# Kernel tuning notes

Hardware: AMD Instinct MI355X
Metric: run time of the kernel (lower is better)

## Reference

```python
import jax, jax.numpy as jnp
import numpy as np

D = 20          # embedding dim (hardcoded in original module)
N_REL = 200     # relation vocab size (table has N_REL+1 rows)
N_TIME = 365    # time embedding table size
L = 3           # propagation layers
E = 2_000_000   # edges per layer
N = 1_000_000   # node-slot pool per layer
B = 64          # batch size
N_ENT = 1_000_003


def setup_inputs() -> dict:
    key = jax.random.key(0)
    ks = jax.random.split(key, 16)
    src_idx = jax.random.randint(ks[0], (L, E), 0, N, dtype=jnp.int32)
    dst_idx = jax.random.randint(ks[1], (L, E), 0, N, dtype=jnp.int32)
    rel_idx = jax.random.randint(ks[2], (L, E), 0, N_REL + 1, dtype=jnp.int32)
    qrel_idx = jax.random.randint(ks[3], (L, E), 0, N_REL + 1, dtype=jnp.int32)
    # signed relative time (edge_time - query_time); abs() must stay < N_TIME
    rel_time = jax.random.randint(ks[4], (L, E), -(N_TIME - 1), N_TIME, dtype=jnp.int32)
    node_batch = jax.random.randint(ks[5], (N,), 0, B, dtype=jnp.int32)
    node_ent = jnp.arange(N, dtype=jnp.int32)  # unique entity per final node slot
    s = 0.1
    rela_embed = jax.random.normal(ks[6], (N_REL + 1, D), jnp.float32) * s
    time_embed = jax.random.normal(ks[7], (N_TIME, D), jnp.float32) * s
    w_att1 = jax.random.normal(ks[8], (30, 3 * D), jnp.float32) * s
    w_att2 = jax.random.normal(ks[9], (1, 30), jnp.float32) * s
    w_past = jax.random.normal(ks[10], (D, D), jnp.float32) * s
    w_now = jax.random.normal(ks[11], (D, D), jnp.float32) * s
    w_future = jax.random.normal(ks[12], (D, D), jnp.float32) * s
    w_cls = jax.random.normal(ks[13], (D,), jnp.float32) * s
    b_cls = jnp.zeros((), jnp.float32)
    return dict(src_idx=src_idx, dst_idx=dst_idx, rel_idx=rel_idx,
                qrel_idx=qrel_idx, rel_time=rel_time, node_batch=node_batch,
                node_ent=node_ent, rela_embed=rela_embed, time_embed=time_embed,
                w_att1=w_att1, w_att2=w_att2, w_past=w_past, w_now=w_now,
                w_future=w_future, w_cls=w_cls, b_cls=b_cls,
                batch_size=B, n_ent=N_ENT)


def reference(src_idx, dst_idx, rel_idx, qrel_idx, rel_time, node_batch,
              node_ent, rela_embed, time_embed, w_att1, w_att2, w_past,
              w_now, w_future, w_cls, b_cls, batch_size, n_ent):
    n_layers = src_idx.shape[0]
    n_nodes = node_batch.shape[0]
    d = rela_embed.shape[1]
    hidden = jnp.zeros((n_nodes, d), dtype=rela_embed.dtype)
    for l in range(n_layers):
        rt = rel_time[l]                         # [E] signed relative time
        h_src = hidden[src_idx[l]]               # [E, D] gather
        r_emb = rela_embed[rel_idx[l]]           # [E, D]
        t_emb = time_embed[jnp.abs(rt)]          # [E, D]
        embed_rel = h_src + r_emb + t_emb
        # conditional time-branch MLP (mask-partitioned linear, same math as
        # the original's boolean-masked assignments)
        fut = embed_rel @ w_future.T
        now = embed_rel @ w_now.T
        pst = embed_rel @ w_past.T
        transformed = jnp.where((rt > 0)[:, None], fut,
                       jnp.where((rt == 0)[:, None], now, pst))
        # attention over concat(hidden_src, rel_emb, query_rel_emb)  [E, 3D]
        att_in = jnp.concatenate([h_src, r_emb, rela_embed[qrel_idx[l]]], axis=1)
        score = jax.nn.sigmoid(jax.nn.relu(att_in @ w_att1.T) @ w_att2.T)  # [E,1]
        msg = score * transformed                # [E, D]
        hidden = jax.ops.segment_sum(msg, dst_idx[l], num_segments=n_nodes)
        hidden = jax.nn.leaky_relu(hidden)       # default slope 0.01, as torch
    result = hidden @ w_cls + b_cls              # [N]
    score_all = jnp.zeros((batch_size, n_ent), dtype=result.dtype)
    score_all = score_all.at[node_batch, node_ent].set(result)
    return score_all
```

## Files before the change

kernel.cpp:

```cpp
#include <hip/hip_runtime.h>
#include <hip/hip_bf16.h>
#include <cstdint>

#define DD 20
#define HID 30
#define NB_SCAN 1024
#define MROW 21

typedef unsigned int  u32;
typedef unsigned short u16;

__device__ __forceinline__ void load20(const float* __restrict__ p, float* r){
  const float4* q = (const float4*)p;
#pragma unroll
  for (int i=0;i<5;i++){ float4 v=q[i]; r[4*i+0]=v.x; r[4*i+1]=v.y; r[4*i+2]=v.z; r[4*i+3]=v.w; }
}

__global__ void k_prep(const float* __restrict__ rela, const float* __restrict__ w1,
                       const float* __restrict__ wp, const float* __restrict__ wn,
                       const float* __restrict__ wf,
                       float* __restrict__ W3, float* __restrict__ AR, float* __restrict__ AQ,
                       int nrel){
  int t = blockIdx.x*blockDim.x + threadIdx.x;
  if (t < 3*DD*DD){
    int s = t/(DD*DD), idx = t%(DD*DD);
    W3[t] = (s==0)?wp[idx]:((s==1)?wn[idx]:wf[idx]);
  }
  if (t < nrel*HID){
    int r=t/HID, j=t-r*HID;
    float sr=0.f, sq=0.f;
#pragma unroll
    for (int k=0;k<DD;k++){
      float e = rela[r*DD+k];
      sr += e*w1[j*3*DD + DD + k];
      sq += e*w1[j*3*DD + 2*DD + k];
    }
    AR[r*32+j]=sr; AQ[r*32+j]=sq;
  }
}

__global__ void k_rwtw(const float* __restrict__ rela, const float* __restrict__ timee,
                       const float* __restrict__ W3,
                       float* __restrict__ RW, float* __restrict__ TW,
                       int nrel, int ntime){
  int t = blockIdx.x*blockDim.x+threadIdx.x;
  int totR = 3*nrel*DD, totT = 3*ntime*DD;
  if (t < totR){
    int sel = t/(nrel*DD); int rem = t - sel*nrel*DD; int r = rem/DD; int i = rem - r*DD;
    const float* w = W3 + sel*DD*DD + i*DD;
    const float* e = rela + (size_t)r*DD;
    float s=0.f;
#pragma unroll
    for (int k=0;k<DD;k++) s += e[k]*w[k];
    RW[t]=s;
  }
  if (t < totT){
    int sel = t/(ntime*DD); int rem = t - sel*ntime*DD; int tt = rem/DD; int i = rem - tt*DD;
    const float* w = W3 + sel*DD*DD + i*DD;
    const float* e = timee + (size_t)tt*DD;
    float s=0.f;
#pragma unroll
    for (int k=0;k<DD;k++) s += e[k]*w[k];
    TW[t]=s;
  }
}

__global__ void k_rt(const float* __restrict__ rela, const float* __restrict__ timee,
                     const float* __restrict__ W3, float* __restrict__ RT,
                     int nrel, int ntime){
  int row = blockIdx.x*blockDim.x+threadIdx.x;
  int tot = 3*nrel*ntime;
  if (row>=tot) return;
  int per = nrel*ntime;
  int sel = row/per; int rem = row - sel*per; int r = rem/ntime; int t = rem - r*ntime;
  float e[DD], tv[DD];
  load20(rela + (size_t)r*DD, e);
  load20(timee + (size_t)t*DD, tv);
#pragma unroll
  for (int k=0;k<DD;k++) e[k]+=tv[k];
  const float* W = W3 + sel*DD*DD;
  float o[DD];
#pragma unroll
  for (int i=0;i<DD;i++){
    const float4* wr = (const float4*)(W + i*DD);
    float s=0.f;
#pragma unroll
    for (int c=0;c<5;c++){ float4 w=wr[c]; s += e[4*c]*w.x + e[4*c+1]*w.y + e[4*c+2]*w.z + e[4*c+3]*w.w; }
    o[i]=s;
  }
  float4* op=(float4*)(RT + (size_t)row*DD);
#pragma unroll
  for (int c=0;c<5;c++){ float4 v; v.x=o[4*c]; v.y=o[4*c+1]; v.z=o[4*c+2]; v.w=o[4*c+3]; op[c]=v; }
}

__global__ void __launch_bounds__(256) k_pre(const int* __restrict__ dst, int* __restrict__ cnt,
        int* __restrict__ rank, int E, int N,
        float4* __restrict__ dout4, size_t nd4,
        float4* __restrict__ b0, float4* __restrict__ b1, size_t nb4,
        float4* __restrict__ bF, size_t nf4,
        float4* __restrict__ res4, size_t nr4){
  int g=blockIdx.x, tid=threadIdx.x;
  int half=gridDim.x>>1;
  if (g & 1){
    int stride=half*256;
    int E2=2*E;
    for (int e=(g>>1)*256+tid; e<E2; e+=stride){
      int l=(e>=E)?1:0;
      rank[e]=atomicAdd(&cnt[(size_t)l*N+dst[e]],1);
    }
  } else {
    float4 z=make_float4(0.f,0.f,0.f,0.f);
    size_t i=(size_t)(g>>1)*256+tid, st=(size_t)half*256;
    for (size_t k=i;k<nd4;k+=st) dout4[k]=z;
    for (size_t k=i;k<nb4;k+=st){ b0[k]=z; b1[k]=z; }
    for (size_t k=i;k<nf4;k+=st) bF[k]=z;
    for (size_t k=i;k<nr4;k+=st) res4[k]=z;
  }
}

__global__ void k_scan_part(const int* __restrict__ cnt, int* __restrict__ part, int M, int C){
  __shared__ int sm[256];
  int b=blockIdx.x, t=threadIdx.x;
  int lo=b*C, hi=lo+C; if (hi>M) hi=M; if (lo>M) lo=M;
  int s=0;
  for (int i=lo+t; i<hi; i+=256) s+=cnt[i];
  sm[t]=s; __syncthreads();
  for (int o=128;o>0;o>>=1){ if (t<o) sm[t]+=sm[t+o]; __syncthreads(); }
  if (t==0) part[b]=sm[0];
}

__global__ void k_scan_top(int* __restrict__ part, int* __restrict__ listc){
  __shared__ int sm[NB_SCAN];
  int t=threadIdx.x;
  if (t==0) *listc=0;
  int v=part[t]; sm[t]=v; __syncthreads();
  for (int o=1;o<NB_SCAN;o<<=1){
    int u=(t>=o)?sm[t-o]:0; __syncthreads();
    sm[t]+=u; __syncthreads();
  }
  part[t]=sm[t]-v;
}

__global__ void k_scan_write(const int* __restrict__ cnt, const int* __restrict__ part,
                             int* __restrict__ rowptr, int M, int C, int base){
  __shared__ int sm[256];
  int b=blockIdx.x, t=threadIdx.x;
  int lo=b*C, hi=lo+C; if (hi>M) hi=M; if (lo>M) lo=M;
  int run=part[b]+base;
  for (int bb=lo; bb<hi; bb+=256){
    int i=bb+t;
    int v=(i<hi)?cnt[i]:0;
    sm[t]=v; __syncthreads();
    for (int o=1;o<256;o<<=1){
      int u=(t>=o)?sm[t-o]:0; __syncthreads();
      sm[t]+=u; __syncthreads();
    }
    if (i<hi) rowptr[i]=run+sm[t]-v;
    int tot=sm[255];
    __syncthreads();
    run+=tot;
  }
  if (hi==M && t==0) rowptr[M]=run;
}

__global__ void __launch_bounds__(256) k_scat01(const int* __restrict__ src,const int* __restrict__ dst,
  const int* __restrict__ rel,const int* __restrict__ qrel,const int* __restrict__ rtm,
  const int* __restrict__ rank,const int* __restrict__ rowptr,int4* __restrict__ recs,int E,int N){
  int e=blockIdx.x*blockDim.x+threadIdx.x;
  if (e>=2*E) return;
  int l=(e>=E)?1:0;
  int d=dst[e];
  int pos=rowptr[(size_t)l*N+d]+rank[e];
  recs[pos]=make_int4(src[e], rel[e]|(qrel[e]<<16), rtm[e], d);
}

__global__ void __launch_bounds__(256) k_scat2(const int* __restrict__ src,const int* __restrict__ dst,
  const int* __restrict__ rel,const int* __restrict__ qrel,const int* __restrict__ rtm,
  const int* __restrict__ rank,const int* __restrict__ rowptr2,int4* __restrict__ recs,int E){
  int e=blockIdx.x*blockDim.x+threadIdx.x;
  if (e>=E) return;
  int d=dst[e];
  int pos=rowptr2[d]+rank[e];
  recs[pos]=make_int4(src[e], rel[e]|(qrel[e]<<16), rtm[e], d);
}

template<bool HASH,bool FINAL,bool HIST>
__global__ void __launch_bounds__(256) k_fused(
    const int4* __restrict__ recs,
    const float* __restrict__ hin, float* __restrict__ hout, float* __restrict__ bufF,
    const float* __restrict__ RW, const float* __restrict__ TW,
    const float* __restrict__ AR, const float* __restrict__ AQ,
    const float* __restrict__ w1, const float* __restrict__ w2, const float* __restrict__ W3,
    int E, int nrel, int ntime,
    const int* __restrict__ hB_dst, int* __restrict__ hB_cnt, int* __restrict__ hB_rank, int hB_E,
    const float* __restrict__ wcls, float* __restrict__ res,
    int* __restrict__ list, int* __restrict__ listc)
{
  int lb;
  if (HIST){
    int g=blockIdx.x;
    int r3=g%3, b3=g/3;
    if (r3==2){
      int H=gridDim.x/3;
      int stride=H*256;
      for (int e=b3*256+threadIdx.x; e<hB_E; e+=stride)
        hB_rank[e]=atomicAdd(&hB_cnt[hB_dst[e]],1);
      return;
    }
    lb=b3*2+r3;
  } else lb=blockIdx.x;
  int bstart=lb*256;
  if (bstart>=E) return;

  __shared__ float sW1h[HID*DD];
  __shared__ float sW2[32];
  __shared__ float sW3[3*DD*DD];
  __shared__ float smsg[256*MROW];
  __shared__ int   sdst[256];
  __shared__ int   s_prevdst, s_nextdst;
  if (HASH){
    for (int t=threadIdx.x; t<HID*DD; t+=blockDim.x){ int j=t/DD,k=t-j*DD; sW1h[t]=w1[j*3*DD+k]; }
    for (int t=threadIdx.x; t<3*DD*DD; t+=blockDim.x) sW3[t]=W3[t];
  }
  if (threadIdx.x<HID) sW2[threadIdx.x]=w2[threadIdx.x];

  int tid = threadIdx.x;
  int bsize = E - bstart; if (bsize>256) bsize=256;
  int j = bstart + tid;
  bool active = (tid < bsize);

  if (tid==0){
    s_prevdst = (bstart>0) ? recs[-1 + (ptrdiff_t)bstart].w : -1;
    s_nextdst = (bstart+bsize < E) ? recs[bstart+bsize].w : -1;
  }
  __syncthreads();

  int dstv = -1;
  float m[DD];
  if (active){
    int4 rc = recs[j];
    int s = rc.x;
    int r = rc.y & 0xFFFF;
    int q = ((unsigned)rc.y) >> 16;
    int t = rc.z;
    dstv  = rc.w;
    int sel = (t>0)?2:((t==0)?1:0);
    int ta = (t<0)?-t:t;

    float h[DD];
    if (HASH){
      load20(hin+(size_t)s*DD, h);
#pragma unroll
      for (int i=0;i<DD;i++) h[i]=fmaxf(h[i],0.01f*h[i]);
    }

    float z=0.f;
    {
      const float4* ap=(const float4*)(AR+(size_t)r*32);
      const float4* qp=(const float4*)(AQ+(size_t)q*32);
#pragma unroll
      for (int c=0;c<7;c++){
        float4 x=ap[c], y=qp[c];
        float s4[4]={x.x+y.x, x.y+y.y, x.z+y.z, x.w+y.w};
#pragma unroll
        for (int u=0;u<4;u++){
          int jj=4*c+u;
          if (HASH){
            const float4* wr=(const float4*)&sW1h[jj*DD];
            float sum=s4[u];
#pragma unroll
            for (int c2=0;c2<5;c2++){ float4 w=wr[c2]; sum += h[4*c2]*w.x+h[4*c2+1]*w.y+h[4*c2+2]*w.z+h[4*c2+3]*w.w; }
            s4[u]=sum;
          }
          z += fmaxf(s4[u],0.f)*sW2[jj];
        }
      }
      float2 x2=*(const float2*)(AR+(size_t)r*32+28);
      float2 y2=*(const float2*)(AQ+(size_t)q*32+28);
      float s0=x2.x+y2.x, s1=x2.y+y2.y;
      if (HASH){
        const float4* wr0=(const float4*)&sW1h[28*DD];
        const float4* wr1=(const float4*)&sW1h[29*DD];
#pragma unroll
        for (int c2=0;c2<5;c2++){
          float4 wA=wr0[c2], wB=wr1[c2];
          s0 += h[4*c2]*wA.x+h[4*c2+1]*wA.y+h[4*c2+2]*wA.z+h[4*c2+3]*wA.w;
          s1 += h[4*c2]*wB.x+h[4*c2+1]*wB.y+h[4*c2+2]*wB.z+h[4*c2+3]*wB.w;
        }
      }
      z += fmaxf(s0,0.f)*sW2[28] + fmaxf(s1,0.f)*sW2[29];
    }
    float score = 1.f/(1.f+__expf(-z));

    const float4* rwp=(const float4*)(RW + ((size_t)(sel*nrel+r))*DD);
    const float4* twp=(const float4*)(TW + ((size_t)(sel*ntime+ta))*DD);
#pragma unroll
    for (int c=0;c<5;c++){
      float4 a4=rwp[c], b4=twp[c];
      float mv[4]={a4.x+b4.x, a4.y+b4.y, a4.z+b4.z, a4.w+b4.w};
      if (HASH){
#pragma unroll
        for (int u=0;u<4;u++){
          const float4* wr=(const float4*)&sW3[sel*DD*DD+(4*c+u)*DD];
          float sum=mv[u];
#pragma unroll
          for (int c2=0;c2<5;c2++){ float4 w=wr[c2]; sum += h[4*c2]*w.x+h[4*c2+1]*w.y+h[4*c2+2]*w.z+h[4*c2+3]*w.w; }
          mv[u]=sum;
        }
      }
#pragma unroll
      for (int u=0;u<4;u++){ m[4*c+u]=score*mv[u]; smsg[tid*MROW+4*c+u]=m[4*c+u]; }
    }
  }
  sdst[tid] = active ? dstv : -2;
  __syncthreads();

  if (!active) return;
  bool isHead = (tid==0) ? (s_prevdst != dstv) : (sdst[tid-1] != dstv);
  if (!(isHead || tid==0)) return;
  int k=tid+1;
  for (; k<bsize && sdst[k]==dstv; ++k){
    const float* row=&smsg[k*MROW];
#pragma unroll
    for (int i=0;i<DD;i++) m[i]+=row[i];
  }
  bool crossStart = (tid==0 && !isHead);
  bool crossEnd   = (k==bsize) && (s_nextdst==dstv);
  if (crossStart || crossEnd){
    float* o = bufF + (size_t)dstv*DD;
#pragma unroll
    for (int i=0;i<DD;i++) atomicAdd(o+i, m[i]);
    if (!FINAL && isHead){
      int p = atomicAdd(listc,1);
      list[p] = dstv;
    }
  } else {
    if (!FINAL){
      float4* op=(float4*)(hout + (size_t)dstv*DD);
#pragma unroll
      for (int c=0;c<5;c++){ float4 v; v.x=m[4*c]; v.y=m[4*c+1]; v.z=m[4*c+2]; v.w=m[4*c+3]; op[c]=v; }
    } else {
      float rsum=0.f;
#pragma unroll
      for (int i=0;i<DD;i++){ float x=fmaxf(m[i],0.01f*m[i]); rsum += x*wcls[i]; }
      res[dstv] = rsum;
    }
  }
}

__global__ void __launch_bounds__(256) k_fixup(float* __restrict__ bufF, float* __restrict__ hout,
   const int* __restrict__ list,const int* __restrict__ listc){
  int c=*listc;
  for (int i=blockIdx.x*blockDim.x+threadIdx.x; i<c; i+=gridDim.x*blockDim.x){
    int n=list[i];
    float* p=bufF+(size_t)n*DD;
    float* o=hout+(size_t)n*DD;
#pragma unroll
    for (int jj=0;jj<DD;jj++){ o[jj]=p[jj]; p[jj]=0.f; }
  }
}

__global__ void __launch_bounds__(256) k_out(const float* __restrict__ res,
   const float* __restrict__ bufF, const float* __restrict__ wcls, const float* __restrict__ bcls,
   const int* __restrict__ nb, const int* __restrict__ ne, const int* __restrict__ nentp,
   float* __restrict__ out, int N){
  int n=blockIdx.x*blockDim.x+threadIdx.x;
  if (n>=N) return;
  float acc = res[n] + bcls[0];
  const float4* q=(const float4*)(bufF+(size_t)n*DD);
#pragma unroll
  for (int c=0;c<5;c++){
    float4 v=q[c];
    acc += fmaxf(v.x,0.01f*v.x)*wcls[4*c]   + fmaxf(v.y,0.01f*v.y)*wcls[4*c+1]
         + fmaxf(v.z,0.01f*v.z)*wcls[4*c+2] + fmaxf(v.w,0.01f*v.w)*wcls[4*c+3];
  }
  long long stride = nentp[0];
  out[(long long)nb[n]*stride + ne[n]] = acc;
}

template<bool HASH>
__global__ void __launch_bounds__(256) k_edge(
    const int* __restrict__ src, const int* __restrict__ dst,
    const int* __restrict__ rel, const int* __restrict__ qrel,
    const int* __restrict__ rtm,
    const float* __restrict__ hin, float* __restrict__ hout,
    const float* __restrict__ RT, const float* __restrict__ AR, const float* __restrict__ AQ,
    const float* __restrict__ w1, const float* __restrict__ w2, const float* __restrict__ W3,
    int E, int nrel, int ntime)
{
  __shared__ float sW1h[HID*DD];
  __shared__ float sW2[32];
  __shared__ float sW3[3*DD*DD];
  for (int t=threadIdx.x; t<HID*DD; t+=blockDim.x){ int j=t/DD,k=t-j*DD; sW1h[t]=w1[j*3*DD+k]; }
  if (threadIdx.x<HID) sW2[threadIdx.x]=w2[threadIdx.x];
  for (int t=threadIdx.x; t<3*DD*DD; t+=blockDim.x) sW3[t]=W3[t];
  __syncthreads();
  int e = blockIdx.x*blockDim.x+threadIdx.x;
  if (e>=E) return;
  int s=src[e], d=dst[e], r=rel[e], q=qrel[e], t=rtm[e];
  int sel = (t>0)?2:((t==0)?1:0);
  int ta = (t<0)?-t:t;
  float h[DD];
  if (HASH){
    load20(hin+(size_t)s*DD, h);
#pragma unroll
    for (int i=0;i<DD;i++) h[i]=fmaxf(h[i],0.01f*h[i]);
  }
  float a[HID];
  {
    const float4* ap=(const float4*)(AR+(size_t)r*32);
    const float4* qp=(const float4*)(AQ+(size_t)q*32);
#pragma unroll
    for (int c=0;c<7;c++){
      float4 x=ap[c], y=qp[c];
      a[4*c+0]=x.x+y.x; a[4*c+1]=x.y+y.y; a[4*c+2]=x.z+y.z; a[4*c+3]=x.w+y.w;
    }
    float2 x=*(const float2*)(AR+(size_t)r*32+28);
    float2 y=*(const float2*)(AQ+(size_t)q*32+28);
    a[28]=x.x+y.x; a[29]=x.y+y.y;
  }
  if (HASH){
#pragma unroll
    for (int j=0;j<HID;j++){
      const float4* wr=(const float4*)&sW1h[j*DD];
      float sum=a[j];
#pragma unroll
      for (int c=0;c<5;c++){ float4 w=wr[c]; sum += h[4*c]*w.x+h[4*c+1]*w.y+h[4*c+2]*w.z+h[4*c+3]*w.w; }
      a[j]=sum;
    }
  }
  float z=0.f;
#pragma unroll
  for (int j=0;j<HID;j++) z += fmaxf(a[j],0.f)*sW2[j];
  float score = 1.f/(1.f+__expf(-z));
  float tr[DD];
  load20(RT + ((size_t)(sel*nrel+r)*ntime + ta)*DD, tr);
  if (HASH){
    const float* Ws = sW3 + sel*DD*DD;
#pragma unroll
    for (int i=0;i<DD;i++){
      const float4* wr=(const float4*)(Ws+i*DD);
      float sum=tr[i];
#pragma unroll
      for (int c=0;c<5;c++){ float4 w=wr[c]; sum += h[4*c]*w.x+h[4*c+1]*w.y+h[4*c+2]*w.z+h[4*c+3]*w.w; }
      tr[i]=sum;
    }
  }
  float* o = hout + (size_t)d*DD;
#pragma unroll
  for (int i=0;i<DD;i++) atomicAdd(o+i, score*tr[i]);
}

__global__ void k_result(const float* __restrict__ h, const float* __restrict__ wcls,
                         const float* __restrict__ bcls, float* __restrict__ res, int N){
  int i = blockIdx.x*blockDim.x+threadIdx.x;
  if (i>=N) return;
  float acc = bcls[0];
  const float4* q=(const float4*)(h+(size_t)i*DD);
#pragma unroll
  for (int c=0;c<5;c++){
    float4 v=q[c];
    float x0=fmaxf(v.x,0.01f*v.x), x1=fmaxf(v.y,0.01f*v.y);
    float x2=fmaxf(v.z,0.01f*v.z), x3=fmaxf(v.w,0.01f*v.w);
    acc += x0*wcls[4*c]+x1*wcls[4*c+1]+x2*wcls[4*c+2]+x3*wcls[4*c+3];
  }
  res[i]=acc;
}

__global__ void k_scatter(const float* __restrict__ res, const int* __restrict__ nb,
                          const int* __restrict__ ne, const int* __restrict__ nentp,
                          float* __restrict__ out, int N){
  int i=blockIdx.x*blockDim.x+threadIdx.x;
  if (i>=N) return;
  long long stride = nentp[0];
  out[(long long)nb[i]*stride + ne[i]] = res[i];
}

extern "C" void kernel_launch(void* const* d_in, const int* in_sizes, int n_in,
                              void* d_out, int out_size, void* d_ws, size_t ws_size,
                              hipStream_t stream){
  const int*   src =(const int*)d_in[0];
  const int*   dst =(const int*)d_in[1];
  const int*   rel =(const int*)d_in[2];
  const int*   qrel=(const int*)d_in[3];
  const int*   rtm =(const int*)d_in[4];
  const int*   nb  =(const int*)d_in[5];
  const int*   ne  =(const int*)d_in[6];
  const float* rela=(const float*)d_in[7];
  const float* timee=(const float*)d_in[8];
  const float* w1  =(const float*)d_in[9];
  const float* w2  =(const float*)d_in[10];
  const float* wp  =(const float*)d_in[11];
  const float* wn  =(const float*)d_in[12];
  const float* wf  =(const float*)d_in[13];
  const float* wcls=(const float*)d_in[14];
  const float* bcls=(const float*)d_in[15];
  const int*   nentp=(const int*)d_in[17];

  const int Lc=3;
  int LE=in_sizes[0]; int E=LE/Lc;
  int N=in_sizes[5];
  int nrel=in_sizes[7]/DD;
  int ntime=in_sizes[8]/DD;

  auto al=[](size_t x){ return (x+(size_t)255)&~(size_t)255; };
  size_t szBuf =al((size_t)N*DD*4);
  size_t szRW  =al((size_t)3*nrel*DD*4);
  size_t szTW  =al((size_t)3*ntime*DD*4);
  size_t szRTf =al((size_t)3*nrel*ntime*DD*4);
  size_t szA   =al((size_t)nrel*32*4);
  size_t szW3  =al((size_t)3*DD*DD*4);
  size_t szRow =al(((size_t)3*N+3)*4);
  size_t szRank=al((size_t)LE*4);
  size_t szCnt =al((size_t)Lc*N*4);
  size_t szRecs=al((size_t)LE*16);
  size_t szPart=al((size_t)NB_SCAN*4);
  size_t szList=al((size_t)(131072+16)*4);
  size_t szRes =al((size_t)N*4);
  size_t need = 3*szBuf+szRW+szTW+2*szA+szW3+szRow+szRank+szCnt+szRecs+szPart+szList+szRes;

  dim3 blk(256);
  int prepTot = (3*DD*DD > nrel*HID) ? 3*DD*DD : nrel*HID;
  int rtTot=3*nrel*ntime;
  int rwtwTot = 3*ntime*DD;

  if (ws_size >= need){
    char* base=(char*)d_ws;
    size_t off=0;
    float* b0 =(float*)(base+off);  off+=szBuf;
    float* b1 =(float*)(base+off);  off+=szBuf;
    float* bufF=(float*)(base+off); off+=szBuf;
    float* RW  =(float*)(base+off); off+=szRW;
    float* TW  =(float*)(base+off); off+=szTW;
    float* AR  =(float*)(base+off); off+=szA;
    float* AQ  =(float*)(base+off); off+=szA;
    float* W3  =(float*)(base+off); off+=szW3;
    int*   rowptr=(int*)(base+off); off+=szRow;
    int*   rowptr2=rowptr+(size_t)2*N+1;
    int*   rank=(int*)(base+off);  off+=szRank;
    int*   cnt =(int*)(base+off);  off+=szCnt;
    int4*  recs=(int4*)(base+off); off+=szRecs;
    int*   part=(int*)(base+off);  off+=szPart;
    int*   listc=(int*)(base+off);
    int*   list =listc+16;          off+=szList;
    float* res =(float*)(base+off); off+=szRes;

    float* dout=(float*)d_out;

    (void)hipMemsetAsync(cnt,0,(size_t)Lc*N*4,stream);
    k_prep<<<dim3((prepTot+255)/256),blk,0,stream>>>(rela,w1,wp,wn,wf,W3,AR,AQ,nrel);
    k_rwtw<<<dim3((rwtwTot+255)/256),blk,0,stream>>>(rela,timee,W3,RW,TW,nrel,ntime);

    size_t nd4=(size_t)out_size>>2;
    size_t nb4=(size_t)N*DD/4;
    size_t nr4=(size_t)N/4;
    k_pre<<<dim3(8192),blk,0,stream>>>(dst,cnt,rank,E,N,(float4*)dout,nd4,
                                       (float4*)b0,(float4*)b1,nb4,(float4*)bufF,nb4,
                                       (float4*)res,nr4);

    int LB=(E+255)/256;
    int H=(LB+1)/2;

    {
      int M=2*N, C=(M+NB_SCAN-1)/NB_SCAN;
      k_scan_part<<<dim3(NB_SCAN),blk,0,stream>>>(cnt,part,M,C);
      k_scan_top<<<dim3(1),dim3(NB_SCAN),0,stream>>>(part,listc);
      k_scan_write<<<dim3(NB_SCAN),blk,0,stream>>>(cnt,part,rowptr,M,C,0);
    }
    k_scat01<<<dim3((2*E+255)/256),blk,0,stream>>>(src,dst,rel,qrel,rtm,rank,rowptr,recs,E,N);

    k_fused<false,false,true><<<dim3(3*H),blk,0,stream>>>(recs,nullptr,b0,bufF,
        RW,TW,AR,AQ,w1,w2,W3,E,nrel,ntime,
        dst+(size_t)2*E,cnt+(size_t)2*N,rank+(size_t)2*E,E,
        wcls,res,list,listc);
    k_fixup<<<dim3(128),blk,0,stream>>>(bufF,b0,list,listc);

    {
      int C=(N+NB_SCAN-1)/NB_SCAN;
      k_scan_part<<<dim3(NB_SCAN),blk,0,stream>>>(cnt+(size_t)2*N,part,N,C);
      k_scan_top<<<dim3(1),dim3(NB_SCAN),0,stream>>>(part,listc);
      k_scan_write<<<dim3(NB_SCAN),blk,0,stream>>>(cnt+(size_t)2*N,part,rowptr2,N,C,2*E);
    }
    k_scat2<<<dim3(LB),blk,0,stream>>>(src+(size_t)2*E,dst+(size_t)2*E,rel+(size_t)2*E,
        qrel+(size_t)2*E,rtm+(size_t)2*E,rank+(size_t)2*E,rowptr2,recs,E);

    k_fused<true,false,false><<<dim3(LB),blk,0,stream>>>(recs+(size_t)E,b0,b1,bufF,
        RW,TW,AR,AQ,w1,w2,W3,E,nrel,ntime,
        nullptr,nullptr,nullptr,0,
        wcls,res,list,listc);
    k_fixup<<<dim3(128),blk,0,stream>>>(bufF,b1,list,listc);

    k_fused<true,true,false><<<dim3(LB),blk,0,stream>>>(recs+(size_t)2*E,b1,nullptr,bufF,
        RW,TW,AR,AQ,w1,w2,W3,E,nrel,ntime,
        nullptr,nullptr,nullptr,0,
        wcls,res,list,listc);

    k_out<<<dim3((N+255)/256),blk,0,stream>>>(res,bufF,wcls,bcls,nb,ne,nentp,dout,N);
  } else {
    char* base=(char*)d_out; float* res=(float*)d_ws;
    size_t off=0;
    float* buf0=(float*)(base+off); off+=szBuf;
    float* buf1=(float*)(base+off); off+=szBuf;
    float* RT  =(float*)(base+off); off+=szRTf;
    float* AR  =(float*)(base+off); off+=szA;
    float* AQ  =(float*)(base+off); off+=szA;
    float* W3  =(float*)(base+off); off+=szW3;
    k_prep<<<dim3((prepTot+255)/256),blk,0,stream>>>(rela,w1,wp,wn,wf,W3,AR,AQ,nrel);
    k_rt<<<dim3((rtTot+255)/256),blk,0,stream>>>(rela,timee,W3,RT,nrel,ntime);
    dim3 egrid((E+255)/256);
    dim3 ngrid((N+255)/256);
    (void)hipMemsetAsync(buf0,0,(size_t)N*DD*4,stream);
    k_edge<false><<<egrid,blk,0,stream>>>(src,dst,rel,qrel,rtm,nullptr,buf0,RT,AR,AQ,w1,w2,W3,E,nrel,ntime);
    (void)hipMemsetAsync(buf1,0,(size_t)N*DD*4,stream);
    k_edge<true><<<egrid,blk,0,stream>>>(src+(size_t)E,dst+(size_t)E,rel+(size_t)E,qrel+(size_t)E,rtm+(size_t)E,
                                         buf0,buf1,RT,AR,AQ,w1,w2,W3,E,nrel,ntime);
    (void)hipMemsetAsync(buf0,0,(size_t)N*DD*4,stream);
    k_edge<true><<<egrid,blk,0,stream>>>(src+(size_t)2*E,dst+(size_t)2*E,rel+(size_t)2*E,qrel+(size_t)2*E,rtm+(size_t)2*E,
                                         buf1,buf0,RT,AR,AQ,w1,w2,W3,E,nrel,ntime);
    k_result<<<ngrid,blk,0,stream>>>(buf0,wcls,bcls,res,N);
    (void)hipMemsetAsync(d_out,0,(size_t)out_size*sizeof(float),stream);
    k_scatter<<<ngrid,blk,0,stream>>>(res,nb,ne,nentp,(float*)d_out,N);
  }
}
```

Baseline: 1.053 ms.

## Zero only empty node slots during scan and pack segment messages as bf16

Drops the bulk zeroing of the hidden buffers b0/b1 and the result array in k_pre. Instead, the scan-write kernel zeros only the node rows whose in-degree count is zero, relying on every other row being fully written later. Separately, per-edge messages staged in shared memory for the segmented reduction are packed as bf16 pairs, halving LDS footprint, which may raise occupancy. The bf16 rounding of intermediate messages reduces accumulation precision and could affect tolerance.

```diff
diff --git a/kernel.cpp b/kernel.cpp
--- a/kernel.cpp
+++ b/kernel.cpp
@@ -5,7 +5,6 @@
 #define DD 20
 #define HID 30
 #define NB_SCAN 1024
-#define MROW 21
 
 typedef unsigned int  u32;
 typedef unsigned short u16;
@@ -14,6 +13,12 @@
   const float4* q = (const float4*)p;
 #pragma unroll
   for (int i=0;i<5;i++){ float4 v=q[i]; r[4*i+0]=v.x; r[4*i+1]=v.y; r[4*i+2]=v.z; r[4*i+3]=v.w; }
+}
+
+__device__ __forceinline__ u32 pkbf(float a, float b){
+  u32 ua=__float_as_uint(a); ua=(ua+0x7FFFu+((ua>>16)&1u))>>16;
+  u32 ub=__float_as_uint(b); ub=(ub+0x7FFFu+((ub>>16)&1u))>>16;
+  return ua | (ub<<16);
 }
 
 __global__ void k_prep(const float* __restrict__ rela, const float* __restrict__ w1,
@@ -96,9 +101,7 @@
 __global__ void __launch_bounds__(256) k_pre(const int* __restrict__ dst, int* __restrict__ cnt,
         int* __restrict__ rank, int E, int N,
         float4* __restrict__ dout4, size_t nd4,
-        float4* __restrict__ b0, float4* __restrict__ b1, size_t nb4,
-        float4* __restrict__ bF, size_t nf4,
-        float4* __restrict__ res4, size_t nr4){
+        float4* __restrict__ bF, size_t nf4){
   int g=blockIdx.x, tid=threadIdx.x;
   int half=gridDim.x>>1;
   if (g & 1){
@@ -112,9 +115,7 @@
     float4 z=make_float4(0.f,0.f,0.f,0.f);
     size_t i=(size_t)(g>>1)*256+tid, st=(size_t)half*256;
     for (size_t k=i;k<nd4;k+=st) dout4[k]=z;
-    for (size_t k=i;k<nb4;k+=st){ b0[k]=z; b1[k]=z; }
     for (size_t k=i;k<nf4;k+=st) bF[k]=z;
-    for (size_t k=i;k<nr4;k+=st) res4[k]=z;
   }
 }
 
@@ -141,8 +142,11 @@
   part[t]=sm[t]-v;
 }
 
+template<int ZM>
 __global__ void k_scan_write(const int* __restrict__ cnt, const int* __restrict__ part,
-                             int* __restrict__ rowptr, int M, int C, int base){
+                             int* __restrict__ rowptr, int M, int C, int base,
+                             float* __restrict__ zb0, float* __restrict__ zb1, int Nsplit,
+                             float* __restrict__ zres){
   __shared__ int sm[256];
   int b=blockIdx.x, t=threadIdx.x;
   int lo=b*C, hi=lo+C; if (hi>M) hi=M; if (lo>M) lo=M;
@@ -150,6 +154,17 @@
   for (int bb=lo; bb<hi; bb+=256){
     int i=bb+t;
     int v=(i<hi)?cnt[i]:0;
+    if (i<hi && v==0){
+      if (ZM==1){
+        float* o=(i<Nsplit)? zb0+(size_t)i*DD : zb1+(size_t)(i-Nsplit)*DD;
+        float4 z=make_float4(0.f,0.f,0.f,0.f);
+        float4* o4=(float4*)o;
+#pragma unroll
+        for (int c=0;c<5;c++) o4[c]=z;
+      } else if (ZM==2){
+        zres[i]=0.f;
+      }
+    }
     sm[t]=v; __syncthreads();
     for (int o=1;o<256;o<<=1){
       int u=(t>=o)?sm[t-o]:0; __syncthreads();
@@ -215,7 +230,7 @@
   __shared__ float sW1h[HID*DD];
   __shared__ float sW2[32];
   __shared__ float sW3[3*DD*DD];
-  __shared__ float smsg[256*MROW];
+  __shared__ u32   smsg[256*10];
   __shared__ int   sdst[256];
   __shared__ int   s_prevdst, s_nextdst;
   if (HASH){
@@ -309,7 +324,9 @@
         }
       }
 #pragma unroll
-      for (int u=0;u<4;u++){ m[4*c+u]=score*mv[u]; smsg[tid*MROW+4*c+u]=m[4*c+u]; }
+      for (int u=0;u<4;u++) m[4*c+u]=score*mv[u];
+      smsg[tid*10+2*c]  =pkbf(m[4*c+0],m[4*c+1]);
+      smsg[tid*10+2*c+1]=pkbf(m[4*c+2],m[4*c+3]);
     }
   }
   sdst[tid] = active ? dstv : -2;
@@ -320,9 +337,13 @@
   if (!(isHead || tid==0)) return;
   int k=tid+1;
   for (; k<bsize && sdst[k]==dstv; ++k){
-    const float* row=&smsg[k*MROW];
-#pragma unroll
-    for (int i=0;i<DD;i++) m[i]+=row[i];
+    const u32* row=&smsg[k*10];
+#pragma unroll
+    for (int i2=0;i2<10;i2++){
+      u32 w=row[i2];
+      m[2*i2]  +=__uint_as_float(w<<16);
+      m[2*i2+1]+=__uint_as_float(w&0xFFFF0000u);
+    }
   }
   bool crossStart = (tid==0 && !isHead);
   bool crossEnd   = (k==bsize) && (s_nextdst==dstv);
@@ -553,10 +574,8 @@
 
     size_t nd4=(size_t)out_size>>2;
     size_t nb4=(size_t)N*DD/4;
-    size_t nr4=(size_t)N/4;
     k_pre<<<dim3(8192),blk,0,stream>>>(dst,cnt,rank,E,N,(float4*)dout,nd4,
-                                       (float4*)b0,(float4*)b1,nb4,(float4*)bufF,nb4,
-                                       (float4*)res,nr4);
+                                       (float4*)bufF,nb4);
 
     int LB=(E+255)/256;
     int H=(LB+1)/2;
@@ -565,7 +584,7 @@
       int M=2*N, C=(M+NB_SCAN-1)/NB_SCAN;
       k_scan_part<<<dim3(NB_SCAN),blk,0,stream>>>(cnt,part,M,C);
       k_scan_top<<<dim3(1),dim3(NB_SCAN),0,stream>>>(part,listc);
-      k_scan_write<<<dim3(NB_SCAN),blk,0,stream>>>(cnt,part,rowptr,M,C,0);
+      k_scan_write<1><<<dim3(NB_SCAN),blk,0,stream>>>(cnt,part,rowptr,M,C,0,b0,b1,N,nullptr);
     }
     k_scat01<<<dim3((2*E+255)/256),blk,0,stream>>>(src,dst,rel,qrel,rtm,rank,rowptr,recs,E,N);
 
@@ -579,7 +598,8 @@
       int C=(N+NB_SCAN-1)/NB_SCAN;
       k_scan_part<<<dim3(NB_SCAN),blk,0,stream>>>(cnt+(size_t)2*N,part,N,C);
       k_scan_top<<<dim3(1),dim3(NB_SCAN),0,stream>>>(part,listc);
-      k_scan_write<<<dim3(NB_SCAN),blk,0,stream>>>(cnt+(size_t)2*N,part,rowptr2,N,C,2*E);
+      k_scan_write<2><<<dim3(NB_SCAN),blk,0,stream>>>(cnt+(size_t)2*N,part,rowptr2,N,C,2*E,
+                                                      nullptr,nullptr,0,res);
     }
     k_scat2<<<dim3(LB),blk,0,stream>>>(src+(size_t)2*E,dst+(size_t)2*E,rel+(size_t)2*E,
         qrel+(size_t)2*E,rtm+(size_t)2*E,rank+(size_t)2*E,rowptr2,recs,E);
```

Result: no change. 1.046 ms (-0.7%).
